# Kernel tuning notes

Measured on AMD Instinct MI355X. Metric: run time of the kernel, lower is better.

The kernel has to match this reference:

```python
import jax, jax.numpy as jnp
import numpy as np

B, L1, NF, L2, IMG, H, N, D, L3, CA = 1, 10752, 21, 769, 257, 1536, 12, 128, 32, 768
EPS = 1e-6


def rms_norm(x, w):
    # WanRMSNorm: normalize in fp32 over last dim, scale by learned weight
    v = jnp.mean(jnp.square(x.astype(jnp.float32)), axis=-1, keepdims=True)
    return (x.astype(jnp.float32) * jax.lax.rsqrt(v + EPS)).astype(x.dtype) * w


def masked_attention(q, k, v, k_lens=None):
    # q: [b, Lq, n, d]; k, v: [b, Lk, n, d]; k_lens: [b] or None
    scale = 1.0 / jnp.sqrt(jnp.asarray(q.shape[-1], q.dtype))
    s = jnp.einsum('bqnd,bknd->bnqk', q, k) * scale
    if k_lens is not None:
        mask = jnp.arange(k.shape[1])[None, None, None, :] < k_lens[:, None, None, None]
        s = jnp.where(mask, s, jnp.asarray(-1e30, s.dtype))
    p = jax.nn.softmax(s, axis=-1)
    return jnp.einsum('bnqk,bknd->bqnd', p, v)


def setup_inputs() -> dict:
    key = jax.random.key(0)
    ks = jax.random.split(key, 24)
    sd = 0.02
    inp = {
        'x': jax.random.normal(ks[0], (B, L1, H), jnp.float32),
        'context': jax.random.normal(ks[1], (B, L2, H), jnp.float32),
        'audio_proj': jax.random.normal(ks[2], (B, NF, L3, CA), jnp.float32),
        'Wq': jax.random.normal(ks[3], (H, H), jnp.float32) * sd,
        'bq': jnp.zeros((H,), jnp.float32),
        'Wk': jax.random.normal(ks[4], (H, H), jnp.float32) * sd,
        'bk': jnp.zeros((H,), jnp.float32),
        'Wv': jax.random.normal(ks[5], (H, H), jnp.float32) * sd,
        'bv': jnp.zeros((H,), jnp.float32),
        'Wk_img': jax.random.normal(ks[6], (H, H), jnp.float32) * sd,
        'bk_img': jnp.zeros((H,), jnp.float32),
        'Wv_img': jax.random.normal(ks[7], (H, H), jnp.float32) * sd,
        'bv_img': jnp.zeros((H,), jnp.float32),
        'Wo': jax.random.normal(ks[8], (H, H), jnp.float32) * sd,
        'bo': jnp.zeros((H,), jnp.float32),
        'norm_q_w': jnp.ones((H,), jnp.float32),
        'norm_k_w': jnp.ones((H,), jnp.float32),
        'norm_k_img_w': jnp.ones((H,), jnp.float32),
        'Wkp': jax.random.normal(ks[9], (H, CA), jnp.float32) * sd,  # zero-init in src; randomized for testing
        'Wvp': jax.random.normal(ks[10], (H, CA), jnp.float32) * sd,
        'context_lens': jnp.maximum(jax.random.randint(ks[11], (B,), 0, 513), 256).astype(jnp.int32),
        'audio_context_lens': jnp.maximum(jax.random.randint(ks[12], (B * NF,), 0, L3 + 1), 8).astype(jnp.int32),
    }
    return inp


def reference(x, context, audio_proj, Wq, bq, Wk, bk, Wv, bv, Wk_img, bk_img,
              Wv_img, bv_img, Wo, bo, norm_q_w, norm_k_w, norm_k_img_w,
              Wkp, Wvp, context_lens, audio_context_lens):
    audio_scale = 1.0
    context_img = context[:, :IMG]
    context_txt = context[:, IMG:]
    b = x.shape[0]

    q = rms_norm(x @ Wq.T + bq, norm_q_w).reshape(b, -1, N, D)
    k = rms_norm(context_txt @ Wk.T + bk, norm_k_w).reshape(b, -1, N, D)
    v = (context_txt @ Wv.T + bv).reshape(b, -1, N, D)
    k_img = rms_norm(context_img @ Wk_img.T + bk_img, norm_k_img_w).reshape(b, -1, N, D)
    v_img = (context_img @ Wv_img.T + bv_img).reshape(b, -1, N, D)

    img_x = masked_attention(q, k_img, v_img, k_lens=None).reshape(b, -1, N * D)
    txt_x = masked_attention(q, k, v, k_lens=context_lens).reshape(b, -1, N * D)

    # audio branch (audio_proj is 4D): per-frame cross attention
    audio_q = q.reshape(b * NF, -1, N, D)                      # [b*21, L1/21, n, d]
    ip_key = (audio_proj @ Wkp.T).reshape(b * NF, -1, N, D)
    ip_value = (audio_proj @ Wvp.T).reshape(b * NF, -1, N, D)
    audio_x = masked_attention(audio_q, ip_key, ip_value, k_lens=audio_context_lens)
    audio_x = audio_x.reshape(b, q.shape[1], N * D)

    out = txt_x + img_x + audio_x * audio_scale
    return out @ Wo.T + bo
```

## Files before the change

kernel.cpp:

```cpp
#include <hip/hip_runtime.h>

typedef __bf16 bf16x8 __attribute__((ext_vector_type(8)));
typedef unsigned short u16x8 __attribute__((ext_vector_type(8)));
typedef float f32x4 __attribute__((ext_vector_type(4)));

__device__ __forceinline__ unsigned short f2bf(float f) {
  __bf16 b = (__bf16)f;
  return __builtin_bit_cast(unsigned short, b);
}

__device__ __forceinline__ f32x4 mfma16(u16x8 a, u16x8 b, f32x4 c) {
  return __builtin_amdgcn_mfma_f32_16x16x32_bf16(
      __builtin_bit_cast(bf16x8, a), __builtin_bit_cast(bf16x8, b), c, 0, 0, 0);
}

#define GLD16(gp, lp)                                                              \
  __builtin_amdgcn_global_load_lds((const __attribute__((address_space(1))) void*)(gp), \
                                   (__attribute__((address_space(3))) void*)(lp), 16, 0, 0)

struct CJobs {
  const float* s[11];
  unsigned short* d[11];
  int n4[11];
};
__global__ __launch_bounds__(256) void k_convN(CJobs j) {
  const int job = blockIdx.y;
  const int n4 = j.n4[job];
  const float* __restrict__ src = j.s[job];
  unsigned short* __restrict__ dst = j.d[job];
  for (int i = blockIdx.x * 256 + threadIdx.x; i < n4; i += gridDim.x * 256) {
    float4 v = ((const float4*)src)[i];
    ushort4 o;
    o.x = f2bf(v.x); o.y = f2bf(v.y); o.z = f2bf(v.z); o.w = f2bf(v.w);
    ((ushort4*)dst)[i] = o;
  }
}

__global__ __launch_bounds__(512, 2) void k_gemm256(const unsigned short* __restrict__ A,
                                                    const unsigned short* __restrict__ B,
                                                    float* __restrict__ C,
                                                    int M, int N, int K,
                                                    const float* __restrict__ bias) {
  __shared__ unsigned short lA[2][256 * 64];
  __shared__ unsigned short lB[2][256 * 64];
  const int tid = threadIdx.x;
  const int l = tid & 63, w = tid >> 6;
  const int wm = w >> 2, wn = w & 3;
  const int lr = l & 15, lg = l >> 4;
  const int m0 = blockIdx.y * 256, n0 = blockIdx.x * 256;

  const int srow = tid >> 3;
  const int g8 = ((tid & 7) ^ (srow & 7)) * 8;
  const unsigned short* pA = A + (long)(m0 + srow) * K + g8;
  const unsigned short* pB = B + (long)(n0 + srow) * K + g8;
  const long iStrA = (long)64 * K;

  const int rdA = (wm * 128 + lr) * 64;
  const int rdB = (wn * 64 + lr) * 64;
  const int ck[2] = { (lg ^ (lr & 7)) * 8, ((4 + lg) ^ (lr & 7)) * 8 };

  const f32x4 zero4 = {0.f, 0.f, 0.f, 0.f};
  f32x4 acc[8][4];
#pragma unroll
  for (int i = 0; i < 8; i++)
#pragma unroll
    for (int j = 0; j < 4; j++) acc[i][j] = zero4;

  const int NT = K >> 6;

#pragma unroll
  for (int i = 0; i < 4; i++) GLD16(pA + i * iStrA, &lA[0][(i * 512 + w * 64) * 8]);
#pragma unroll
  for (int i = 0; i < 4; i++) GLD16(pB + i * iStrA, &lB[0][(i * 512 + w * 64) * 8]);
  pA += 64; pB += 64;

  int cur = 0;
  for (int t = 0; t < NT; t++) {
    if (t + 1 < NT) {
      const int b = cur ^ 1;
#pragma unroll
      for (int i = 0; i < 4; i++) GLD16(pA + i * iStrA, &lA[b][(i * 512 + w * 64) * 8]);
#pragma unroll
      for (int i = 0; i < 4; i++) GLD16(pB + i * iStrA, &lB[b][(i * 512 + w * 64) * 8]);
      pA += 64; pB += 64;
      __builtin_amdgcn_sched_barrier(0);
      asm volatile("s_waitcnt vmcnt(8)" ::: "memory");
    } else {
      __builtin_amdgcn_sched_barrier(0);
      asm volatile("s_waitcnt vmcnt(0)" ::: "memory");
    }
    __builtin_amdgcn_sched_barrier(0);
    __builtin_amdgcn_s_barrier();

    const unsigned short* lAc = lA[cur];
    const unsigned short* lBc = lB[cur];
#pragma unroll
    for (int ks = 0; ks < 2; ks++) {
      u16x8 a8[8], b4[4];
#pragma unroll
      for (int mb = 0; mb < 8; mb++)
        a8[mb] = *(const u16x8*)(lAc + rdA + mb * 16 * 64 + ck[ks]);
#pragma unroll
      for (int nb = 0; nb < 4; nb++)
        b4[nb] = *(const u16x8*)(lBc + rdB + nb * 16 * 64 + ck[ks]);
#pragma unroll
      for (int mb = 0; mb < 8; mb++)
#pragma unroll
        for (int nb = 0; nb < 4; nb++) acc[mb][nb] = mfma16(a8[mb], b4[nb], acc[mb][nb]);
    }
    __builtin_amdgcn_sched_barrier(0);
    __builtin_amdgcn_s_barrier();
    cur ^= 1;
  }

#pragma unroll
  for (int mb = 0; mb < 8; mb++)
#pragma unroll
    for (int nb = 0; nb < 4; nb++) {
      const int col = n0 + wn * 64 + nb * 16 + lr;
      const float bv = bias[col];
#pragma unroll
      for (int r = 0; r < 4; r++) {
        const int row = m0 + wm * 128 + mb * 16 + lg * 4 + r;
        C[(long)row * N + col] = acc[mb][nb][r] + bv;
      }
    }
}

struct GJob {
  const unsigned short* A; const unsigned short* B;
  float* Cf; unsigned short* CKbf; unsigned short* CVT;
  int NK, M, K, nbx, bstart;
  const float* bias0; const float* bias1;
};
struct GJobs { GJob j[3]; };

__global__ __launch_bounds__(256) void k_gemm_small(GJobs js) {
  const int bid = blockIdx.x;
  const int ji = (bid >= js.j[1].bstart) + (bid >= js.j[2].bstart);
  const GJob J = js.j[ji];
  const int rel = bid - J.bstart;
  const int m0 = (rel / J.nbx) * 128, n0 = (rel % J.nbx) * 128;
  const int M = J.M, K = J.K;
  const int N = 3072;

  __shared__ unsigned short lA[128 * 32];
  __shared__ unsigned short lB[128 * 32];
  const int tid = threadIdx.x;
  const int l = tid & 63, w = tid >> 6;
  const int wm = w >> 1, wn = w & 1;
  const int lr = l & 15, lg = l >> 4;

  const int srow = w * 16 + (l >> 2);
  const int sk8 = (l & 3) * 8;
  int raA0 = m0 + srow;       if (raA0 >= M) raA0 = M - 1;
  int raA1 = m0 + 64 + srow;  if (raA1 >= M) raA1 = M - 1;
  const long rbB0 = (long)(n0 + srow) * K;
  const long rbB1 = (long)(n0 + 64 + srow) * K;
  const long raA0o = (long)raA0 * K, raA1o = (long)raA1 * K;
  unsigned short* ldsA0 = &lA[(w * 16) * 32];
  unsigned short* ldsA1 = &lA[(64 + w * 16) * 32];
  unsigned short* ldsB0 = &lB[(w * 16) * 32];
  unsigned short* ldsB1 = &lB[(64 + w * 16) * 32];

  const f32x4 zero4 = {0.f, 0.f, 0.f, 0.f};
  f32x4 acc[4][4];
#pragma unroll
  for (int i = 0; i < 4; i++)
#pragma unroll
    for (int j = 0; j < 4; j++) acc[i][j] = zero4;

  for (int k0 = 0; k0 < K; k0 += 32) {
    __syncthreads();
    GLD16(J.A + raA0o + k0 + sk8, ldsA0);
    GLD16(J.A + raA1o + k0 + sk8, ldsA1);
    GLD16(J.B + rbB0 + k0 + sk8, ldsB0);
    GLD16(J.B + rbB1 + k0 + sk8, ldsB1);
    __syncthreads();

    u16x8 af[4], bfr[4];
#pragma unroll
    for (int mb = 0; mb < 4; mb++)
      af[mb] = *(const u16x8*)(&lA[(wm * 64 + mb * 16 + lr) * 32 + lg * 8]);
#pragma unroll
    for (int nb = 0; nb < 4; nb++)
      bfr[nb] = *(const u16x8*)(&lB[(wn * 64 + nb * 16 + lr) * 32 + lg * 8]);
#pragma unroll
    for (int mb = 0; mb < 4; mb++)
#pragma unroll
      for (int nb = 0; nb < 4; nb++) acc[mb][nb] = mfma16(af[mb], bfr[nb], acc[mb][nb]);
  }

#pragma unroll
  for (int mb = 0; mb < 4; mb++)
#pragma unroll
    for (int nb = 0; nb < 4; nb++)
#pragma unroll
      for (int r = 0; r < 4; r++) {
        int row = m0 + wm * 64 + mb * 16 + lg * 4 + r;
        if (row < M) {
          int col = n0 + wn * 64 + nb * 16 + lr;
          float b = 0.f;
          if (col < 1536) { if (J.bias0) b = J.bias0[col]; }
          else            { if (J.bias1) b = J.bias1[col - 1536]; }
          float val = acc[mb][nb][r] + b;
          if (col < 1536) {
            if (J.CKbf) J.CKbf[(long)row * 1536 + col] = f2bf(val);
            else        J.Cf[(long)row * 1536 + col] = val;
          } else {
            int c2 = col - 1536, hh = c2 >> 7, dd = c2 & 127;
            long addr = (J.NK == 32)
                ? ((((long)(row >> 5) * 12 + hh) * 128 + dd) * 32 + (row & 31))
                : (((long)hh * 128 + dd) * J.NK + row);
            J.CVT[addr] = f2bf(val);
          }
        }
      }
}

struct PJob { const float* src; const float* w; unsigned short* dst; float pscale; int rstart; };
struct PJobs { PJob j[3]; };
__global__ __launch_bounds__(256) void k_postproc(PJobs js) {
  const int bid = blockIdx.x;
  const int ji = (bid >= js.j[1].rstart) + (bid >= js.j[2].rstart);
  const PJob J = js.j[ji];
  const int row = bid - J.rstart;
  const float* s = J.src + (long)row * 1536;
  float v[6];
  float ss = 0.f;
#pragma unroll
  for (int i = 0; i < 6; i++) {
    v[i] = s[threadIdx.x + i * 256];
    ss += v[i] * v[i];
  }
#pragma unroll
  for (int o = 1; o < 64; o <<= 1) ss += __shfl_xor(ss, o, 64);
  __shared__ float red[4];
  if ((threadIdx.x & 63) == 0) red[threadIdx.x >> 6] = ss;
  __syncthreads();
  float tot = red[0] + red[1] + red[2] + red[3];
  float scale = rsqrtf(tot * (1.f / 1536.f) + 1e-6f) * J.pscale;
  unsigned short* d = J.dst + (long)row * 1536;
#pragma unroll
  for (int i = 0; i < 6; i++)
    d[threadIdx.x + i * 256] = f2bf(v[i] * scale * J.w[threadIdx.x + i * 256]);
}

__global__ __launch_bounds__(256) void k_attn(
    const unsigned short* __restrict__ qb, const unsigned short* __restrict__ kt,
    const unsigned short* __restrict__ vtT, const unsigned short* __restrict__ ki,
    const unsigned short* __restrict__ viT, const unsigned short* __restrict__ ka,
    const unsigned short* __restrict__ vaT, const int* __restrict__ clen_p,
    const int* __restrict__ alens, unsigned short* __restrict__ out) {
  __shared__ unsigned short lK[2][32 * 128];
  __shared__ unsigned short lV[2][128 * 32];
  __shared__ unsigned short lP[4][16 * 40];

  const int qt = blockIdx.x, h = blockIdx.y;
  const int tid = threadIdx.x, l = tid & 63, w = tid >> 6;
  const int lr = l & 15, lg = l >> 4;
  const int q0 = qt * 64;
  const int frame = qt >> 3;

  const int key0 = tid >> 4;
  const int swc8 = ((tid & 15) ^ (key0 & 7)) * 8;
  const int d0 = tid >> 2;
  const int kc8 = (tid & 3) * 8;

  u16x8 qf[4];
  {
    const unsigned short* qp = qb + (long)(q0 + w * 16 + lr) * 1536 + h * 128;
#pragma unroll
    for (int kk = 0; kk < 4; kk++) qf[kk] = *(const u16x8*)(qp + kk * 32 + lg * 8);
  }

  const f32x4 zero4 = {0.f, 0.f, 0.f, 0.f};
  f32x4 osum[8];
#pragma unroll
  for (int nb = 0; nb < 8; nb++) osum[nb] = zero4;

  for (int ph = 0; ph < 3; ph++) {
    const unsigned short *kp, *vtp;
    int klen, NK;
    if (ph == 0) {
      kp = ki; vtp = viT + (long)h * 128 * 288; klen = 257; NK = 288;
    } else if (ph == 1) {
      kp = kt; vtp = vtT + (long)h * 128 * 512; klen = clen_p[0]; NK = 512;
    } else {
      kp = ka + (long)frame * 32 * 1536;
      vtp = vaT + (long)frame * 49152 + h * 4096;
      klen = alens[frame]; NK = 32;
    }

    const unsigned short* pk0 = kp + (long)key0 * 1536 + h * 128 + swc8;
    const unsigned short* pk1 = pk0 + 16 * 1536;
    const unsigned short* pv0 = vtp + (long)d0 * NK + kc8;
    const unsigned short* pv1 = pv0 + (long)64 * NK;

    float mloc = -1e30f, lseloc = 0.f;
    f32x4 oacc[8];
#pragma unroll
    for (int nb = 0; nb < 8; nb++) oacc[nb] = zero4;

    const int nt = (klen + 31) >> 5;

    GLD16(pk0, &lK[0][(w * 64) * 8]);
    GLD16(pk1, &lK[0][(256 + w * 64) * 8]);
    GLD16(pv0, &lV[0][(w * 64) * 8]);
    GLD16(pv1, &lV[0][(256 + w * 64) * 8]);
    pk0 += 32 * 1536; pk1 += 32 * 1536; pv0 += 32; pv1 += 32;

    int cur = 0;
    for (int t = 0; t < nt; t++) {
      const int kb0 = t * 32;
      if (t + 1 < nt) {
        const int b = cur ^ 1;
        GLD16(pk0, &lK[b][(w * 64) * 8]);
        GLD16(pk1, &lK[b][(256 + w * 64) * 8]);
        GLD16(pv0, &lV[b][(w * 64) * 8]);
        GLD16(pv1, &lV[b][(256 + w * 64) * 8]);
        pk0 += 32 * 1536; pk1 += 32 * 1536; pv0 += 32; pv1 += 32;
        __builtin_amdgcn_sched_barrier(0);
        asm volatile("s_waitcnt vmcnt(4)" ::: "memory");
      } else {
        __builtin_amdgcn_sched_barrier(0);
        asm volatile("s_waitcnt vmcnt(0)" ::: "memory");
      }
      __builtin_amdgcn_sched_barrier(0);
      __builtin_amdgcn_s_barrier();

      const unsigned short* lKc = &lK[cur][0];
      const unsigned short* lVc = &lV[cur][0];

      f32x4 s0 = zero4, s1 = zero4;
      __builtin_amdgcn_s_setprio(1);
#pragma unroll
      for (int kk = 0; kk < 4; kk++) {
        int c = (kk * 4 + lg) ^ (lr & 7);
        u16x8 k0f = *(const u16x8*)(lKc + lr * 128 + c * 8);
        u16x8 k1f = *(const u16x8*)(lKc + (16 + lr) * 128 + c * 8);
        s0 = mfma16(k0f, qf[kk], s0);
        s1 = mfma16(k1f, qf[kk], s1);
      }
      __builtin_amdgcn_s_setprio(0);

      float p0[4], p1[4];
      if (kb0 + 32 <= klen) {
#pragma unroll
        for (int r = 0; r < 4; r++) { p0[r] = s0[r]; p1[r] = s1[r]; }
      } else {
#pragma unroll
        for (int r = 0; r < 4; r++) {
          p0[r] = (kb0 + lg * 4 + r < klen) ? s0[r] : -1e30f;
          p1[r] = (kb0 + 16 + lg * 4 + r < klen) ? s1[r] : -1e30f;
        }
      }
      float pm = fmaxf(fmaxf(fmaxf(p0[0], p0[1]), fmaxf(p0[2], p0[3])),
                       fmaxf(fmaxf(p1[0], p1[1]), fmaxf(p1[2], p1[3])));
      pm = fmaxf(pm, __shfl_xor(pm, 16, 64));
      pm = fmaxf(pm, __shfl_xor(pm, 32, 64));

      if (__any(pm > mloc + 8.f)) {
        float mn = fmaxf(mloc, pm);
        float alpha = __expf(mloc - mn);
        mloc = mn;
        lseloc *= alpha;
        float aq[4];
#pragma unroll
        for (int r = 0; r < 4; r++) aq[r] = __shfl(alpha, lg * 4 + r, 64);
#pragma unroll
        for (int nb = 0; nb < 8; nb++)
#pragma unroll
          for (int r = 0; r < 4; r++) oacc[nb][r] *= aq[r];
      }
      float rs = 0.f;
#pragma unroll
      for (int r = 0; r < 4; r++) {
        p0[r] = __expf(p0[r] - mloc);
        p1[r] = __expf(p1[r] - mloc);
        rs += p0[r] + p1[r];
      }
      rs += __shfl_xor(rs, 16, 64);
      rs += __shfl_xor(rs, 32, 64);
      lseloc += rs;

      ushort4 sa, sb;
      sa.x = f2bf(p0[0]); sa.y = f2bf(p0[1]); sa.z = f2bf(p0[2]); sa.w = f2bf(p0[3]);
      sb.x = f2bf(p1[0]); sb.y = f2bf(p1[1]); sb.z = f2bf(p1[2]); sb.w = f2bf(p1[3]);
      *(ushort4*)(&lP[w][lr * 40 + lg * 4]) = sa;
      *(ushort4*)(&lP[w][lr * 40 + 16 + lg * 4]) = sb;
      u16x8 pa = *(const u16x8*)(&lP[w][lr * 40 + lg * 8]);

      __builtin_amdgcn_s_setprio(1);
#pragma unroll
      for (int nb = 0; nb < 8; nb++) {
        u16x8 vf = *(const u16x8*)(lVc + (nb * 16 + lr) * 32 + lg * 8);
        oacc[nb] = mfma16(pa, vf, oacc[nb]);
      }
      __builtin_amdgcn_s_setprio(0);

      __builtin_amdgcn_s_barrier();
      cur ^= 1;
    }

    float invl = 1.f / lseloc;
    float inv[4];
#pragma unroll
    for (int r = 0; r < 4; r++) inv[r] = __shfl(invl, lg * 4 + r, 64);
#pragma unroll
    for (int nb = 0; nb < 8; nb++)
#pragma unroll
      for (int r = 0; r < 4; r++) osum[nb][r] += oacc[nb][r] * inv[r];
  }

#pragma unroll
  for (int nb = 0; nb < 8; nb++)
#pragma unroll
    for (int r = 0; r < 4; r++)
      out[(long)(q0 + w * 16 + lg * 4 + r) * 1536 + h * 128 + nb * 16 + lr] =
          f2bf(osum[nb][r]);
}

extern "C" void kernel_launch(void* const* d_in, const int* in_sizes, int n_in,
                              void* d_out, int out_size, void* d_ws, size_t ws_size,
                              hipStream_t stream) {
  (void)in_sizes; (void)n_in; (void)out_size; (void)ws_size;
  const float* x    = (const float*)d_in[0];
  const float* ctx  = (const float*)d_in[1];
  const float* aud  = (const float*)d_in[2];
  const float* Wq   = (const float*)d_in[3];
  const float* bq   = (const float*)d_in[4];
  const float* Wk   = (const float*)d_in[5];
  const float* bk   = (const float*)d_in[6];
  const float* Wv   = (const float*)d_in[7];
  const float* bv   = (const float*)d_in[8];
  const float* Wki  = (const float*)d_in[9];
  const float* bki  = (const float*)d_in[10];
  const float* Wvi  = (const float*)d_in[11];
  const float* bvi  = (const float*)d_in[12];
  const float* Wo   = (const float*)d_in[13];
  const float* bo   = (const float*)d_in[14];
  const float* nqw  = (const float*)d_in[15];
  const float* nkw  = (const float*)d_in[16];
  const float* nkiw = (const float*)d_in[17];
  const float* Wkp  = (const float*)d_in[18];
  const float* Wvp  = (const float*)d_in[19];
  const int* clen   = (const int*)d_in[20];
  const int* alens  = (const int*)d_in[21];
  float* out = (float*)d_out;

  char* ws = (char*)d_ws;
  size_t o = 0;
  auto alloc = [&](size_t bytes) { char* p = ws + o; o += bytes; return p; };
  unsigned short* x_bf    = (unsigned short*)alloc(33030144);
  unsigned short* ctx_bf  = (unsigned short*)alloc(2362368);
  unsigned short* aud_bf  = (unsigned short*)alloc(1032192);
  unsigned short* Wq_bf   = (unsigned short*)alloc(4718592);
  unsigned short* Wo_bf   = (unsigned short*)alloc(4718592);
  unsigned short* Wkv_bf  = (unsigned short*)alloc(9437184);
  unsigned short* Wkvi_bf = (unsigned short*)alloc(9437184);
  unsigned short* Wkva_bf = (unsigned short*)alloc(4718592);
  float* q_f32   = (float*)alloc(66060288);
  float* kvt_f32 = (float*)alloc(3145728);
  float* kvi_f32 = (float*)alloc(1579008);
  unsigned short* q_bf  = (unsigned short*)alloc(33030144);
  unsigned short* kt_bf = (unsigned short*)alloc(1572864);
  unsigned short* ki_bf = (unsigned short*)alloc(884736);
  unsigned short* ka_bf = (unsigned short*)alloc(2064384);
  unsigned short* vtT   = (unsigned short*)alloc(1572864);
  unsigned short* viT   = (unsigned short*)alloc(884736);
  unsigned short* vaT   = (unsigned short*)alloc(2064384);
  unsigned short* attn_bf = x_bf;

  CJobs cj;
  cj.s[0] = x;    cj.d[0] = x_bf;                       cj.n4[0] = 10752 * 1536 / 4;
  cj.s[1] = ctx;  cj.d[1] = ctx_bf;                     cj.n4[1] = 769 * 1536 / 4;
  cj.s[2] = aud;  cj.d[2] = aud_bf;                     cj.n4[2] = 672 * 768 / 4;
  cj.s[3] = Wq;   cj.d[3] = Wq_bf;                      cj.n4[3] = 1536 * 1536 / 4;
  cj.s[4] = Wo;   cj.d[4] = Wo_bf;                      cj.n4[4] = 1536 * 1536 / 4;
  cj.s[5] = Wk;   cj.d[5] = Wkv_bf;                     cj.n4[5] = 1536 * 1536 / 4;
  cj.s[6] = Wv;   cj.d[6] = Wkv_bf + 1536 * 1536;       cj.n4[6] = 1536 * 1536 / 4;
  cj.s[7] = Wki;  cj.d[7] = Wkvi_bf;                    cj.n4[7] = 1536 * 1536 / 4;
  cj.s[8] = Wvi;  cj.d[8] = Wkvi_bf + 1536 * 1536;      cj.n4[8] = 1536 * 1536 / 4;
  cj.s[9] = Wkp;  cj.d[9] = Wkva_bf;                    cj.n4[9] = 1536 * 768 / 4;
  cj.s[10] = Wvp; cj.d[10] = Wkva_bf + 1536 * 768;      cj.n4[10] = 1536 * 768 / 4;
  k_convN<<<dim3(1024, 11), 256, 0, stream>>>(cj);

  k_gemm256<<<dim3(6, 42), 512, 0, stream>>>(x_bf, Wq_bf, q_f32, 10752, 1536, 1536, bq);

  GJobs gj;
  gj.j[0] = { ctx_bf + 257 * 1536, Wkv_bf, kvt_f32, nullptr, vtT, 512, 512, 1536, 24, 0, bk, bv };
  gj.j[1] = { ctx_bf, Wkvi_bf, kvi_f32, nullptr, viT, 288, 257, 1536, 24, 96, bki, bvi };
  gj.j[2] = { aud_bf, Wkva_bf, nullptr, ka_bf, vaT, 32, 672, 768, 24, 168, nullptr, nullptr };
  k_gemm_small<<<312, 256, 0, stream>>>(gj);

  PJobs pj;
  pj.j[0] = { q_f32, nqw, q_bf, 0.08838834764831845f, 0 };
  pj.j[1] = { kvt_f32, nkw, kt_bf, 1.0f, 10752 };
  pj.j[2] = { kvi_f32, nkiw, ki_bf, 1.0f, 11264 };
  k_postproc<<<11521, 256, 0, stream>>>(pj);

  k_attn<<<dim3(168, 12), 256, 0, stream>>>(q_bf, kt_bf, vtT, ki_bf, viT, ka_bf, vaT,
                                            clen, alens, attn_bf);

  k_gemm256<<<dim3(6, 42), 512, 0, stream>>>(attn_bf, Wo_bf, out, 10752, 1536, 1536, bo);
}
```

Before: 492.8 us.

## Widen attention key tiles, emit bf16 Q from GEMM, remap GEMM blocks per XCD

The attention kernel now processes 64 keys per tile instead of 32, with swizzled V layout and exp2-based softmax (log2e folded into the Q norm scale). The Q projection GEMM writes bf16 directly and a dedicated vectorized q-norm kernel replaces the fp32 postprocess for Q, halving that intermediate traffic. GEMM launches use a 1D grid with XCD-aware block remapping to improve L2 locality. The image K/V padding changes to 320 to fit the larger tile. This adds LDS use and register pressure in attention, and rounds Q to bf16 before normalization.

```diff
diff --git a/kernel.cpp b/kernel.cpp
--- a/kernel.cpp
+++ b/kernel.cpp
@@ -7,6 +7,15 @@
 __device__ __forceinline__ unsigned short f2bf(float f) {
   __bf16 b = (__bf16)f;
   return __builtin_bit_cast(unsigned short, b);
+}
+__device__ __forceinline__ float bf2f(unsigned short u) {
+  unsigned v = ((unsigned)u) << 16;
+  return __builtin_bit_cast(float, v);
+}
+__device__ __forceinline__ float fexp2(float x) {
+  float r;
+  asm("v_exp_f32 %0, %1" : "=v"(r) : "v"(x));
+  return r;
 }
 
 __device__ __forceinline__ f32x4 mfma16(u16x8 a, u16x8 b, f32x4 c) {
@@ -38,7 +47,8 @@
 
 __global__ __launch_bounds__(512, 2) void k_gemm256(const unsigned short* __restrict__ A,
                                                     const unsigned short* __restrict__ B,
-                                                    float* __restrict__ C,
+                                                    float* __restrict__ Cf,
+                                                    unsigned short* __restrict__ Cbf,
                                                     int M, int N, int K,
                                                     const float* __restrict__ bias) {
   __shared__ unsigned short lA[2][256 * 64];
@@ -47,7 +57,14 @@
   const int l = tid & 63, w = tid >> 6;
   const int wm = w >> 2, wn = w & 3;
   const int lr = l & 15, lg = l >> 4;
-  const int m0 = blockIdx.y * 256, n0 = blockIdx.x * 256;
+
+  const int nwg = gridDim.x;
+  const int xcd = blockIdx.x & 7, idx = blockIdx.x >> 3;
+  const int q = nwg >> 3, r = nwg & 7;
+  const int start = xcd < r ? xcd * (q + 1) : r * (q + 1) + (xcd - r) * q;
+  const int lb = start + idx;
+  const int ntx = N >> 8;
+  const int m0 = (lb / ntx) * 256, n0 = (lb % ntx) * 256;
 
   const int srow = tid >> 3;
   const int g8 = ((tid & 7) ^ (srow & 7)) * 8;
@@ -120,9 +137,11 @@
       const int col = n0 + wn * 64 + nb * 16 + lr;
       const float bv = bias[col];
 #pragma unroll
-      for (int r = 0; r < 4; r++) {
-        const int row = m0 + wm * 128 + mb * 16 + lg * 4 + r;
-        C[(long)row * N + col] = acc[mb][nb][r] + bv;
+      for (int r2 = 0; r2 < 4; r2++) {
+        const int row = m0 + wm * 128 + mb * 16 + lg * 4 + r2;
+        const float val = acc[mb][nb][r2] + bv;
+        if (Cbf) Cbf[(long)row * N + col] = f2bf(val);
+        else     Cf[(long)row * N + col] = val;
       }
     }
 }
@@ -142,7 +161,6 @@
   const int rel = bid - J.bstart;
   const int m0 = (rel / J.nbx) * 128, n0 = (rel % J.nbx) * 128;
   const int M = J.M, K = J.K;
-  const int N = 3072;
 
   __shared__ unsigned short lA[128 * 32];
   __shared__ unsigned short lB[128 * 32];
@@ -218,11 +236,34 @@
       }
 }
 
-struct PJob { const float* src; const float* w; unsigned short* dst; float pscale; int rstart; };
-struct PJobs { PJob j[3]; };
+__global__ __launch_bounds__(192) void k_qnorm(const unsigned short* __restrict__ src,
+                                               const float* __restrict__ w,
+                                               unsigned short* __restrict__ dst) {
+  const int row = blockIdx.x;
+  u16x8 v = *(const u16x8*)(src + (long)row * 1536 + threadIdx.x * 8);
+  float f[8];
+  float ss = 0.f;
+#pragma unroll
+  for (int j = 0; j < 8; j++) { f[j] = bf2f(v[j]); ss += f[j] * f[j]; }
+#pragma unroll
+  for (int o = 1; o < 64; o <<= 1) ss += __shfl_xor(ss, o, 64);
+  __shared__ float red[3];
+  if ((threadIdx.x & 63) == 0) red[threadIdx.x >> 6] = ss;
+  __syncthreads();
+  float tot = red[0] + red[1] + red[2];
+  float scale = rsqrtf(tot * (1.f / 1536.f) + 1e-6f) * 0.1275174271f;
+  const float* wp = w + threadIdx.x * 8;
+  u16x8 o8;
+#pragma unroll
+  for (int j = 0; j < 8; j++) o8[j] = f2bf(f[j] * scale * wp[j]);
+  *(u16x8*)(dst + (long)row * 1536 + threadIdx.x * 8) = o8;
+}
+
+struct PJob { const float* src; const float* w; unsigned short* dst; int rstart; };
+struct PJobs { PJob j[2]; };
 __global__ __launch_bounds__(256) void k_postproc(PJobs js) {
   const int bid = blockIdx.x;
-  const int ji = (bid >= js.j[1].rstart) + (bid >= js.j[2].rstart);
+  const int ji = (bid >= js.j[1].rstart);
   const PJob J = js.j[ji];
   const int row = bid - J.rstart;
   const float* s = J.src + (long)row * 1536;
@@ -239,7 +280,7 @@
   if ((threadIdx.x & 63) == 0) red[threadIdx.x >> 6] = ss;
   __syncthreads();
   float tot = red[0] + red[1] + red[2] + red[3];
-  float scale = rsqrtf(tot * (1.f / 1536.f) + 1e-6f) * J.pscale;
+  float scale = rsqrtf(tot * (1.f / 1536.f) + 1e-6f);
   unsigned short* d = J.dst + (long)row * 1536;
 #pragma unroll
   for (int i = 0; i < 6; i++)
@@ -252,9 +293,9 @@
     const unsigned short* __restrict__ viT, const unsigned short* __restrict__ ka,
     const unsigned short* __restrict__ vaT, const int* __restrict__ clen_p,
     const int* __restrict__ alens, unsigned short* __restrict__ out) {
-  __shared__ unsigned short lK[2][32 * 128];
-  __shared__ unsigned short lV[2][128 * 32];
-  __shared__ unsigned short lP[4][16 * 40];
+  __shared__ unsigned short lK[2][64 * 128];
+  __shared__ unsigned short lV[2][128 * 64];
+  __shared__ unsigned short lP[4][16 * 72];
 
   const int qt = blockIdx.x, h = blockIdx.y;
   const int tid = threadIdx.x, l = tid & 63, w = tid >> 6;
@@ -262,10 +303,10 @@
   const int q0 = qt * 64;
   const int frame = qt >> 3;
 
-  const int key0 = tid >> 4;
-  const int swc8 = ((tid & 15) ^ (key0 & 7)) * 8;
-  const int d0 = tid >> 2;
-  const int kc8 = (tid & 3) * 8;
+  const int kkey = tid >> 4;
+  const int kchunk = ((tid & 15) ^ (kkey & 7)) * 8;
+  const int vd = tid >> 3;
+  const int vchunk = ((tid & 7) ^ (vd & 7)) * 8;
 
   u16x8 qf[4];
   {
@@ -281,47 +322,47 @@
 
   for (int ph = 0; ph < 3; ph++) {
     const unsigned short *kp, *vtp;
-    int klen, NK;
+    int klen;
+    long vis;
     if (ph == 0) {
-      kp = ki; vtp = viT + (long)h * 128 * 288; klen = 257; NK = 288;
+      kp = ki; vtp = viT + (long)h * 128 * 320; klen = 257; vis = 32 * 320;
     } else if (ph == 1) {
-      kp = kt; vtp = vtT + (long)h * 128 * 512; klen = clen_p[0]; NK = 512;
+      kp = kt; vtp = vtT + (long)h * 128 * 512; klen = clen_p[0]; vis = 32 * 512;
     } else {
       kp = ka + (long)frame * 32 * 1536;
       vtp = vaT + (long)frame * 49152 + h * 4096;
-      klen = alens[frame]; NK = 32;
+      klen = alens[frame]; vis = 32 * 32;
     }
-
-    const unsigned short* pk0 = kp + (long)key0 * 1536 + h * 128 + swc8;
-    const unsigned short* pk1 = pk0 + 16 * 1536;
-    const unsigned short* pv0 = vtp + (long)d0 * NK + kc8;
-    const unsigned short* pv1 = pv0 + (long)64 * NK;
+    const long vNK = vis >> 5;
+
+    const unsigned short* pk = kp + (long)kkey * 1536 + h * 128 + kchunk;
+    const unsigned short* pv = vtp + (long)vd * vNK + vchunk;
 
     float mloc = -1e30f, lseloc = 0.f;
     f32x4 oacc[8];
 #pragma unroll
     for (int nb = 0; nb < 8; nb++) oacc[nb] = zero4;
 
-    const int nt = (klen + 31) >> 5;
-
-    GLD16(pk0, &lK[0][(w * 64) * 8]);
-    GLD16(pk1, &lK[0][(256 + w * 64) * 8]);
-    GLD16(pv0, &lV[0][(w * 64) * 8]);
-    GLD16(pv1, &lV[0][(256 + w * 64) * 8]);
-    pk0 += 32 * 1536; pk1 += 32 * 1536; pv0 += 32; pv1 += 32;
+    const int nt = (klen + 63) >> 6;
+
+#pragma unroll
+    for (int i = 0; i < 4; i++) GLD16(pk + i * 24576, &lK[0][(i * 256 + w * 64) * 8]);
+#pragma unroll
+    for (int i = 0; i < 4; i++) GLD16(pv + i * vis, &lV[0][(i * 256 + w * 64) * 8]);
+    pk += 64 * 1536; pv += 64;
 
     int cur = 0;
     for (int t = 0; t < nt; t++) {
-      const int kb0 = t * 32;
+      const int kb0 = t * 64;
       if (t + 1 < nt) {
         const int b = cur ^ 1;
-        GLD16(pk0, &lK[b][(w * 64) * 8]);
-        GLD16(pk1, &lK[b][(256 + w * 64) * 8]);
-        GLD16(pv0, &lV[b][(w * 64) * 8]);
-        GLD16(pv1, &lV[b][(256 + w * 64) * 8]);
-        pk0 += 32 * 1536; pk1 += 32 * 1536; pv0 += 32; pv1 += 32;
+#pragma unroll
+        for (int i = 0; i < 4; i++) GLD16(pk + i * 24576, &lK[b][(i * 256 + w * 64) * 8]);
+#pragma unroll
+        for (int i = 0; i < 4; i++) GLD16(pv + i * vis, &lV[b][(i * 256 + w * 64) * 8]);
+        pk += 64 * 1536; pv += 64;
         __builtin_amdgcn_sched_barrier(0);
-        asm volatile("s_waitcnt vmcnt(4)" ::: "memory");
+        asm volatile("s_waitcnt vmcnt(8)" ::: "memory");
       } else {
         __builtin_amdgcn_sched_barrier(0);
         asm volatile("s_waitcnt vmcnt(0)" ::: "memory");
@@ -332,37 +373,45 @@
       const unsigned short* lKc = &lK[cur][0];
       const unsigned short* lVc = &lV[cur][0];
 
-      f32x4 s0 = zero4, s1 = zero4;
+      f32x4 s[4];
+#pragma unroll
+      for (int kb = 0; kb < 4; kb++) s[kb] = zero4;
       __builtin_amdgcn_s_setprio(1);
 #pragma unroll
       for (int kk = 0; kk < 4; kk++) {
-        int c = (kk * 4 + lg) ^ (lr & 7);
-        u16x8 k0f = *(const u16x8*)(lKc + lr * 128 + c * 8);
-        u16x8 k1f = *(const u16x8*)(lKc + (16 + lr) * 128 + c * 8);
-        s0 = mfma16(k0f, qf[kk], s0);
-        s1 = mfma16(k1f, qf[kk], s1);
+        const int c = ((kk * 4 + lg) ^ (lr & 7)) * 8;
+#pragma unroll
+        for (int kb = 0; kb < 4; kb++) {
+          u16x8 kf = *(const u16x8*)(lKc + (kb * 16 + lr) * 128 + c);
+          s[kb] = mfma16(kf, qf[kk], s[kb]);
+        }
       }
       __builtin_amdgcn_s_setprio(0);
 
-      float p0[4], p1[4];
-      if (kb0 + 32 <= klen) {
-#pragma unroll
-        for (int r = 0; r < 4; r++) { p0[r] = s0[r]; p1[r] = s1[r]; }
+      float p[4][4];
+      if (kb0 + 64 <= klen) {
+#pragma unroll
+        for (int kb = 0; kb < 4; kb++)
+#pragma unroll
+          for (int r = 0; r < 4; r++) p[kb][r] = s[kb][r];
       } else {
 #pragma unroll
-        for (int r = 0; r < 4; r++) {
-          p0[r] = (kb0 + lg * 4 + r < klen) ? s0[r] : -1e30f;
-          p1[r] = (kb0 + 16 + lg * 4 + r < klen) ? s1[r] : -1e30f;
-        }
-      }
-      float pm = fmaxf(fmaxf(fmaxf(p0[0], p0[1]), fmaxf(p0[2], p0[3])),
-                       fmaxf(fmaxf(p1[0], p1[1]), fmaxf(p1[2], p1[3])));
+        for (int kb = 0; kb < 4; kb++)
+#pragma unroll
+          for (int r = 0; r < 4; r++)
+            p[kb][r] = (kb0 + kb * 16 + lg * 4 + r < klen) ? s[kb][r] : -1e30f;
+      }
+      float pm = -1e30f;
+#pragma unroll
+      for (int kb = 0; kb < 4; kb++)
+#pragma unroll
+        for (int r = 0; r < 4; r++) pm = fmaxf(pm, p[kb][r]);
       pm = fmaxf(pm, __shfl_xor(pm, 16, 64));
       pm = fmaxf(pm, __shfl_xor(pm, 32, 64));
 
       if (__any(pm > mloc + 8.f)) {
         float mn = fmaxf(mloc, pm);
-        float alpha = __expf(mloc - mn);
+        float alpha = fexp2(mloc - mn);
         mloc = mn;
         lseloc *= alpha;
         float aq[4];
@@ -375,27 +424,34 @@
       }
       float rs = 0.f;
 #pragma unroll
-      for (int r = 0; r < 4; r++) {
-        p0[r] = __expf(p0[r] - mloc);
-        p1[r] = __expf(p1[r] - mloc);
-        rs += p0[r] + p1[r];
-      }
+      for (int kb = 0; kb < 4; kb++)
+#pragma unroll
+        for (int r = 0; r < 4; r++) {
+          p[kb][r] = fexp2(p[kb][r] - mloc);
+          rs += p[kb][r];
+        }
       rs += __shfl_xor(rs, 16, 64);
       rs += __shfl_xor(rs, 32, 64);
       lseloc += rs;
 
-      ushort4 sa, sb;
-      sa.x = f2bf(p0[0]); sa.y = f2bf(p0[1]); sa.z = f2bf(p0[2]); sa.w = f2bf(p0[3]);
-      sb.x = f2bf(p1[0]); sb.y = f2bf(p1[1]); sb.z = f2bf(p1[2]); sb.w = f2bf(p1[3]);
-      *(ushort4*)(&lP[w][lr * 40 + lg * 4]) = sa;
-      *(ushort4*)(&lP[w][lr * 40 + 16 + lg * 4]) = sb;
-      u16x8 pa = *(const u16x8*)(&lP[w][lr * 40 + lg * 8]);
+#pragma unroll
+      for (int kb = 0; kb < 4; kb++) {
+        ushort4 s4;
+        s4.x = f2bf(p[kb][0]); s4.y = f2bf(p[kb][1]);
+        s4.z = f2bf(p[kb][2]); s4.w = f2bf(p[kb][3]);
+        *(ushort4*)(&lP[w][lr * 72 + kb * 16 + lg * 4]) = s4;
+      }
+      u16x8 pa0 = *(const u16x8*)(&lP[w][lr * 72 + lg * 8]);
+      u16x8 pa1 = *(const u16x8*)(&lP[w][lr * 72 + 32 + lg * 8]);
 
       __builtin_amdgcn_s_setprio(1);
 #pragma unroll
       for (int nb = 0; nb < 8; nb++) {
-        u16x8 vf = *(const u16x8*)(lVc + (nb * 16 + lr) * 32 + lg * 8);
-        oacc[nb] = mfma16(pa, vf, oacc[nb]);
+        const int row = (nb * 16 + lr) * 64;
+        u16x8 vf0 = *(const u16x8*)(lVc + row + ((lg ^ (lr & 7)) * 8));
+        u16x8 vf1 = *(const u16x8*)(lVc + row + (((4 + lg) ^ (lr & 7)) * 8));
+        oacc[nb] = mfma16(pa0, vf0, oacc[nb]);
+        oacc[nb] = mfma16(pa1, vf1, oacc[nb]);
       }
       __builtin_amdgcn_s_setprio(0);
 
@@ -460,16 +516,17 @@
   unsigned short* Wkv_bf  = (unsigned short*)alloc(9437184);
   unsigned short* Wkvi_bf = (unsigned short*)alloc(9437184);
   unsigned short* Wkva_bf = (unsigned short*)alloc(4718592);
-  float* q_f32   = (float*)alloc(66060288);
+  unsigned short* q_raw = (unsigned short*)alloc(33030144);
   float* kvt_f32 = (float*)alloc(3145728);
   float* kvi_f32 = (float*)alloc(1579008);
   unsigned short* q_bf  = (unsigned short*)alloc(33030144);
   unsigned short* kt_bf = (unsigned short*)alloc(1572864);
-  unsigned short* ki_bf = (unsigned short*)alloc(884736);
-  unsigned short* ka_bf = (unsigned short*)alloc(2064384);
+  unsigned short* ki_bf = (unsigned short*)alloc(983040);
+  unsigned short* ka_bf = (unsigned short*)alloc(2162688);
   unsigned short* vtT   = (unsigned short*)alloc(1572864);
-  unsigned short* viT   = (unsigned short*)alloc(884736);
+  unsigned short* viT   = (unsigned short*)alloc(983040);
   unsigned short* vaT   = (unsigned short*)alloc(2064384);
+  alloc(262144);
   unsigned short* attn_bf = x_bf;
 
   CJobs cj;
@@ -486,22 +543,23 @@
   cj.s[10] = Wvp; cj.d[10] = Wkva_bf + 1536 * 768;      cj.n4[10] = 1536 * 768 / 4;
   k_convN<<<dim3(1024, 11), 256, 0, stream>>>(cj);
 
-  k_gemm256<<<dim3(6, 42), 512, 0, stream>>>(x_bf, Wq_bf, q_f32, 10752, 1536, 1536, bq);
+  k_gemm256<<<252, 512, 0, stream>>>(x_bf, Wq_bf, nullptr, q_raw, 10752, 1536, 1536, bq);
 
   GJobs gj;
   gj.j[0] = { ctx_bf + 257 * 1536, Wkv_bf, kvt_f32, nullptr, vtT, 512, 512, 1536, 24, 0, bk, bv };
-  gj.j[1] = { ctx_bf, Wkvi_bf, kvi_f32, nullptr, viT, 288, 257, 1536, 24, 96, bki, bvi };
+  gj.j[1] = { ctx_bf, Wkvi_bf, kvi_f32, nullptr, viT, 320, 257, 1536, 24, 96, bki, bvi };
   gj.j[2] = { aud_bf, Wkva_bf, nullptr, ka_bf, vaT, 32, 672, 768, 24, 168, nullptr, nullptr };
   k_gemm_small<<<312, 256, 0, stream>>>(gj);
 
+  k_qnorm<<<10752, 192, 0, stream>>>(q_raw, nqw, q_bf);
+
   PJobs pj;
-  pj.j[0] = { q_f32, nqw, q_bf, 0.08838834764831845f, 0 };
-  pj.j[1] = { kvt_f32, nkw, kt_bf, 1.0f, 10752 };
-  pj.j[2] = { kvi_f32, nkiw, ki_bf, 1.0f, 11264 };
-  k_postproc<<<11521, 256, 0, stream>>>(pj);
+  pj.j[0] = { kvt_f32, nkw, kt_bf, 0 };
+  pj.j[1] = { kvi_f32, nkiw, ki_bf, 512 };
+  k_postproc<<<769, 256, 0, stream>>>(pj);
 
   k_attn<<<dim3(168, 12), 256, 0, stream>>>(q_bf, kt_bf, vtT, ki_bf, viT, ka_bf, vaT,
                                             clen, alens, attn_bf);
 
-  k_gemm256<<<dim3(6, 42), 512, 0, stream>>>(attn_bf, Wo_bf, out, 10752, 1536, 1536, bo);
-}
+  k_gemm256<<<252, 512, 0, stream>>>(attn_bf, Wo_bf, out, nullptr, 10752, 1536, 1536, bo);
+}
```

Result: faster. 473.5 us (-3.9%).
